# Optimization experiments

Hardware: AMD Instinct MI355X
Metric: run time of the kernel (lower is better)

Reference implementation:

```python
import jax, jax.numpy as jnp
import numpy as np

N, E = 50000, 800000
NODE_DIM, EDGE_DIM, TIME_DIM, OUT_DIM, N_HEADS = 128, 64, 16, 128, 4
IN_DIM = NODE_DIM + EDGE_DIM + TIME_DIM  # msg_proj input


def setup_inputs() -> dict:
    key = jax.random.key(0)
    ks = jax.random.split(key, 8)
    x = jax.random.normal(ks[0], (N, NODE_DIM), dtype=jnp.float32)
    edge_index = jax.random.randint(ks[1], (2, E), 0, N, dtype=jnp.int32)
    edge_feat = jax.random.normal(ks[2], (E, EDGE_DIM), dtype=jnp.float32)
    time_deltas = jax.random.uniform(ks[3], (E,), dtype=jnp.float32)
    # parameters
    gammas = jnp.ones((TIME_DIM,), jnp.float32)  # ExponentialTimeDecay init_gamma=1.0
    Wm = 0.02 * jax.random.normal(ks[4], (IN_DIM, OUT_DIM), dtype=jnp.float32)
    bm = jnp.zeros((OUT_DIM,), jnp.float32)
    Wa = 0.02 * jax.random.normal(ks[5], (2 * OUT_DIM, N_HEADS), dtype=jnp.float32)
    ba = jnp.zeros((N_HEADS,), jnp.float32)
    Wo = 0.02 * jax.random.normal(ks[6], (OUT_DIM + NODE_DIM, OUT_DIM), dtype=jnp.float32)
    bo = jnp.zeros((OUT_DIM,), jnp.float32)
    ln_g = jnp.ones((OUT_DIM,), jnp.float32)
    ln_b = jnp.zeros((OUT_DIM,), jnp.float32)
    return {"x": x, "edge_index": edge_index, "edge_feat": edge_feat,
            "time_deltas": time_deltas, "gammas": gammas, "Wm": Wm, "bm": bm,
            "Wa": Wa, "ba": ba, "Wo": Wo, "bo": bo, "ln_g": ln_g, "ln_b": ln_b}


def reference(x, edge_index, edge_feat, time_deltas, gammas, Wm, bm, Wa, ba, Wo, bo, ln_g, ln_b):
    src, dst = edge_index[0], edge_index[1]
    # exponential time decay encoding: (E, TIME_DIM)
    dt = jnp.clip(time_deltas, 0.0)[:, None]
    time_enc = jnp.exp(-jax.nn.softplus(gammas)[None, :] * dt)
    # gather + project messages: (E, OUT_DIM)
    msg_in = jnp.concatenate([x[src], edge_feat, time_enc], axis=-1)
    msgs = msg_in @ Wm + bm
    # edge attention, softmax over ALL edges (dim=0, as in the torch code)
    attn_in = jnp.concatenate([msgs, x[dst]], axis=-1)  # (E, 2*OUT_DIM)
    attn_logits = attn_in @ Wa + ba                      # (E, N_HEADS)
    attn_weight = jnp.mean(jax.nn.softmax(attn_logits, axis=0), axis=-1, keepdims=True)
    weighted = msgs * attn_weight
    # scatter-add into per-node aggregates: (N, OUT_DIM)
    agg = jax.ops.segment_sum(weighted, dst, num_segments=N)
    # output MLP (dropout is identity in eval) + LayerNorm
    out = jax.nn.gelu(jnp.concatenate([agg, x], axis=-1) @ Wo + bo, approximate=False)
    mu = jnp.mean(out, axis=-1, keepdims=True)
    var = jnp.mean((out - mu) ** 2, axis=-1, keepdims=True)
    return (out - mu) / jnp.sqrt(var + 1e-5) * ln_g + ln_b
```

## Files before the change

### kernel.cpp

```cpp
#include <hip/hip_runtime.h>
#include <math.h>

#define N_NODES 50000
#define N_EDGES 800000
#define ND 128
#define ED 64
#define TD 16
#define OD 128
#define NH 4
#define INDIM 208
#define K2DIM 336
#define KPAD 352
#define WTPITCH 360
#define NPAD 50048

#define OFF_A      0ll
#define OFF_EINFO  8808448ll
#define OFF_PERM32 12008448ll
#define OFF_RANK   12808448ll
#define OFF_DENOM  13608448ll
#define OFF_SPG    13608464ll
#define OFF_WFUSE  13608480ll
#define OFF_BFUSE  13609312ll
#define OFF_BMO    13609328ll
#define OFF_XS4    13609456ll
#define OFF_XD4    13809456ll
#define OFF_CNT    14009456ll
#define OFF_START  14059456ll
#define OFF_SW     14109472ll
#define OFF_WT     14159520ll
#define OFF_EFB    14182560ll
#define OFF_XBF    39782560ll
#define WS_FLOATS  42982560ll

typedef __attribute__((ext_vector_type(8))) short short8v;
typedef __attribute__((ext_vector_type(4))) float f32x4;

__device__ inline unsigned short f2bf(float f) {
  unsigned u = __float_as_uint(f);
  unsigned r = (u + 0x7fffu + ((u >> 16) & 1u)) >> 16;
  return (unsigned short)r;
}
__device__ inline float bf2f(unsigned us) {
  return __uint_as_float(us << 16);
}

__global__ void k0_prep(const float* __restrict__ Wm, const float* __restrict__ bm,
                        const float* __restrict__ Wa, const float* __restrict__ ba,
                        const float* __restrict__ Wo, const float* __restrict__ gammas,
                        float* __restrict__ ws) {
  int b = blockIdx.x, j = threadIdx.x;
  unsigned short* Wt = (unsigned short*)(ws + OFF_WT);
  if (b < INDIM) {
    float acc = 0.f;
    for (int m = 0; m < OD; ++m) acc += Wm[b * OD + m] * Wo[m * OD + j];
    Wt[j * WTPITCH + b] = f2bf(acc);
    if (j < NH) {
      float a = 0.f;
      for (int m = 0; m < OD; ++m) a += Wm[b * OD + m] * Wa[m * NH + j];
      ws[OFF_WFUSE + (long)b * NH + j] = a;
    }
  } else if (b < K2DIM) {
    Wt[j * WTPITCH + b] = f2bf(Wo[(OD + b - INDIM) * OD + j]);
  } else {
    if (j < TD) ws[OFF_SPG + j] = log1pf(expf(gammas[j]));
    if (j < NH) {
      float a = ba[j];
      for (int m = 0; m < OD; ++m) a += bm[m] * Wa[m * NH + j];
      ws[OFF_BFUSE + j] = a;
    }
    float a2 = 0.f;
    for (int m = 0; m < OD; ++m) a2 += bm[m] * Wo[m * OD + j];
    ws[OFF_BMO + j] = a2;
    for (int p = K2DIM; p < KPAD; ++p) Wt[j * WTPITCH + p] = 0;
  }
}

__global__ __launch_bounds__(256) void k0b_nodeproj(
    const float* __restrict__ x, const float* __restrict__ Wa,
    float* __restrict__ ws) {
  __shared__ float wf[ND * NH];
  __shared__ float wab[ND * NH];
  int tid = threadIdx.x;
  for (int i = tid; i < ND * NH; i += 256) { wf[i] = ws[OFF_WFUSE + i]; wab[i] = Wa[ND * NH + i]; }
  __syncthreads();
  int lane = tid & 63, wv = tid >> 6;
  long n = (long)blockIdx.x * 4 + wv;
  if (n >= N_NODES) return;
  float v0 = x[n * ND + lane], v1 = x[n * ND + 64 + lane];
  unsigned short* xbf = (unsigned short*)(ws + OFF_XBF);
  xbf[n * ND + lane] = f2bf(v0);
  xbf[n * ND + 64 + lane] = f2bf(v1);
  float s0, s1, s2, s3, d0, d1, d2, d3;
  s0 = v0 * wf[lane * 4 + 0] + v1 * wf[(64 + lane) * 4 + 0];
  s1 = v0 * wf[lane * 4 + 1] + v1 * wf[(64 + lane) * 4 + 1];
  s2 = v0 * wf[lane * 4 + 2] + v1 * wf[(64 + lane) * 4 + 2];
  s3 = v0 * wf[lane * 4 + 3] + v1 * wf[(64 + lane) * 4 + 3];
  d0 = v0 * wab[lane * 4 + 0] + v1 * wab[(64 + lane) * 4 + 0];
  d1 = v0 * wab[lane * 4 + 1] + v1 * wab[(64 + lane) * 4 + 1];
  d2 = v0 * wab[lane * 4 + 2] + v1 * wab[(64 + lane) * 4 + 2];
  d3 = v0 * wab[lane * 4 + 3] + v1 * wab[(64 + lane) * 4 + 3];
  for (int off = 32; off; off >>= 1) {
    s0 += __shfl_xor(s0, off); s1 += __shfl_xor(s1, off);
    s2 += __shfl_xor(s2, off); s3 += __shfl_xor(s3, off);
    d0 += __shfl_xor(d0, off); d1 += __shfl_xor(d1, off);
    d2 += __shfl_xor(d2, off); d3 += __shfl_xor(d3, off);
  }
  if (lane == 0) {
    reinterpret_cast<float4*>(ws + OFF_XS4)[n] = make_float4(s0, s1, s2, s3);
    reinterpret_cast<float4*>(ws + OFF_XD4)[n] = make_float4(d0, d1, d2, d3);
  }
}

__global__ __launch_bounds__(256) void k_count(const int* __restrict__ ei,
                                               float* __restrict__ ws) {
  int* cnt = reinterpret_cast<int*>(ws + OFF_CNT);
  int* rank = reinterpret_cast<int*>(ws + OFF_RANK);
  for (long e = (long)blockIdx.x * 256 + threadIdx.x; e < N_EDGES;
       e += (long)gridDim.x * 256)
    rank[e] = atomicAdd(&cnt[ei[N_EDGES + e]], 1);
}

__global__ __launch_bounds__(1024) void k_scan(float* __restrict__ ws) {
  const int* cnt = reinterpret_cast<const int*>(ws + OFF_CNT);
  int* startp = reinterpret_cast<int*>(ws + OFF_START);
  __shared__ int wsum[16];
  int tid = threadIdx.x;
  int lo = tid * 49, hi = min(lo + 49, N_NODES);
  int s = 0;
  for (int i = lo; i < hi; ++i) s += cnt[i];
  int lane = tid & 63, wv = tid >> 6;
  int sc = s;
  for (int off = 1; off < 64; off <<= 1) {
    int t = __shfl_up(sc, off);
    if (lane >= off) sc += t;
  }
  if (lane == 63) wsum[wv] = sc;
  __syncthreads();
  if (tid == 0) {
    int run = 0;
    for (int i = 0; i < 16; ++i) { int t = wsum[i]; wsum[i] = run; run += t; }
  }
  __syncthreads();
  int run = wsum[wv] + sc - s;
  for (int i = lo; i < hi; ++i) { startp[i] = run; run += cnt[i]; }
  if (tid == 1023) startp[N_NODES] = run;
}

__global__ __launch_bounds__(256) void k_fill4(const int* __restrict__ ei,
                                               float* __restrict__ ws) {
  const int* startp = reinterpret_cast<const int*>(ws + OFF_START);
  const int* rank = reinterpret_cast<const int*>(ws + OFF_RANK);
  int* perm32 = reinterpret_cast<int*>(ws + OFF_PERM32);
  for (long e = (long)blockIdx.x * 256 + threadIdx.x; e < N_EDGES;
       e += (long)gridDim.x * 256) {
    int d = ei[N_EDGES + e];
    perm32[startp[d] + rank[e]] = (int)e;
  }
}

__global__ __launch_bounds__(256) void k1f(
    const int* __restrict__ ei, const float* __restrict__ ef,
    const float* __restrict__ td, float* __restrict__ ws) {
  __shared__ float wef[ED * NH];
  __shared__ float wte[TD * NH];
  __shared__ float bf[NH];
  __shared__ float spg[TD];
  __shared__ float part[NH];
  int tid = threadIdx.x;
  for (int i = tid; i < ED * NH; i += 256) wef[i] = ws[OFF_WFUSE + ND * NH + i];
  if (tid < TD * NH) wte[tid] = ws[OFF_WFUSE + (ND + ED) * NH + tid];
  if (tid < NH) { bf[tid] = ws[OFF_BFUSE + tid]; part[tid] = 0.f; }
  if (tid < TD) spg[tid] = ws[OFF_SPG + tid];
  __syncthreads();

  int lane = tid & 63;
  int q = lane >> 4, r = lane & 15, h = r & 3;
  long wid = ((long)blockIdx.x * 256 + tid) >> 6;
  long stride = (long)gridDim.x * 16;
  const float4* ef4 = reinterpret_cast<const float4*>(ef);
  const float* xsf = ws + OFF_XS4;
  const float* xdf = ws + OFF_XD4;
  uint2* efb2 = reinterpret_cast<uint2*>(ws + OFF_EFB);
  uint4* einfo4 = reinterpret_cast<uint4*>(ws + OFF_EINFO);

  float wr[16];
#pragma unroll
  for (int i = 0; i < 16; ++i) wr[i] = wef[16 * r + i];
  float spg_r = spg[r];
  float wt0 = wte[r * 4 + 0], wt1 = wte[r * 4 + 1];
  float wt2 = wte[r * 4 + 2], wt3 = wte[r * 4 + 3];
  float bfh = bf[h];
  float p = 0.f;
  int base16 = lane & 48;

  for (long e = wid * 4 + q; e < N_EDGES; e += stride) {
    int s = ei[e];
    int d = ei[N_EDGES + e];
    float dt = fmaxf(td[e], 0.f);
    float4 efv = ef4[e * 16 + r];
    float ls = xsf[4l * s + h];
    float ld = xdf[4l * d + h];
    float te = __expf(-spg_r * dt);
    uint2 eb;
    eb.x = (unsigned)f2bf(efv.x) | ((unsigned)f2bf(efv.y) << 16);
    eb.y = (unsigned)f2bf(efv.z) | ((unsigned)f2bf(efv.w) << 16);
    efb2[e * 16 + r] = eb;
    float a0 = efv.x * wr[0] + efv.y * wr[4] + efv.z * wr[8]  + efv.w * wr[12] + te * wt0;
    float a1 = efv.x * wr[1] + efv.y * wr[5] + efv.z * wr[9]  + efv.w * wr[13] + te * wt1;
    float a2 = efv.x * wr[2] + efv.y * wr[6] + efv.z * wr[10] + efv.w * wr[14] + te * wt2;
    float a3 = efv.x * wr[3] + efv.y * wr[7] + efv.z * wr[11] + efv.w * wr[15] + te * wt3;
    a0 += __shfl_xor(a0, 1); a1 += __shfl_xor(a1, 1);
    a2 += __shfl_xor(a2, 1); a3 += __shfl_xor(a3, 1);
    a0 += __shfl_xor(a0, 2); a1 += __shfl_xor(a1, 2);
    a2 += __shfl_xor(a2, 2); a3 += __shfl_xor(a3, 2);
    float v = a0;
    v = (h == 1) ? a1 : v;
    v = (h == 2) ? a2 : v;
    v = (h == 3) ? a3 : v;
    v += __shfl_xor(v, 4);
    v += __shfl_xor(v, 8);
    float ev = __expf(v + ls + ld + bfh);
    if (r < 4) p += ev;
    float e0 = __shfl(ev, base16 + 0), e1 = __shfl(ev, base16 + 1);
    float e2 = __shfl(ev, base16 + 2), e3 = __shfl(ev, base16 + 3);
    if (r == 0) {
      unsigned dt16 = (unsigned)(dt * 65535.f + 0.5f);
      if (dt16 > 65535u) dt16 = 65535u;
      uint4 pk;
      pk.x = (unsigned)s | (dt16 << 16);
      pk.y = (unsigned)f2bf(e0) | ((unsigned)f2bf(e1) << 16);
      pk.z = (unsigned)f2bf(e2) | ((unsigned)f2bf(e3) << 16);
      pk.w = 0u;
      einfo4[e] = pk;
    }
  }
  p += __shfl_xor(p, 16);
  p += __shfl_xor(p, 32);
  if (lane < 4) atomicAdd(&part[lane], p);
  __syncthreads();
  if (tid < NH) atomicAdd(&ws[OFF_DENOM + tid], part[tid]);
}

__global__ __launch_bounds__(256) void k4a_agg(float* __restrict__ ws) {
  __shared__ float spg_s[TD];
  __shared__ float invs[NH];
  int tid = threadIdx.x;
  if (tid < TD) spg_s[tid] = ws[OFF_SPG + tid];
  if (tid < NH) invs[tid] = 0.25f / ws[OFF_DENOM + tid];
  __syncthreads();
  int lane = tid & 63;
  long wid = (long)blockIdx.x * 4 + (tid >> 6);
  long nw = (long)gridDim.x * 4;
  const int* start = reinterpret_cast<const int*>(ws + OFF_START);
  const int* perm32 = reinterpret_cast<const int*>(ws + OFF_PERM32);
  const uint4* einfo4 = reinterpret_cast<const uint4*>(ws + OFF_EINFO);
  unsigned short* A = (unsigned short*)(ws + OFF_A);
  const unsigned short* xbf = (const unsigned short*)(ws + OFF_XBF);
  const unsigned short* efb = (const unsigned short*)(ws + OFF_EFB);
  float spg_l = spg_s[lane & 15];
  float inv0 = invs[0], inv1 = invs[1], inv2 = invs[2], inv3 = invs[3];

  for (long n = wid; n < N_NODES; n += nw) {
    int i0 = start[n], i1 = start[n + 1];
    float a0 = 0.f, a1 = 0.f, a2 = 0.f, a3 = 0.f, asw = 0.f;
    for (int base = i0; base < i1; base += 64) {
      int m = min(64, i1 - base);
      int eidx = 0;
      if (lane < m) eidx = perm32[base + lane];
      uint4 pk = einfo4[eidx];
      int j = 0;
      for (; j + 4 <= m; j += 4) {
        unsigned xu[4], eu[4], zu[4], wu[4];
#pragma unroll
        for (int u = 0; u < 4; ++u) {
          xu[u] = (unsigned)__shfl((int)pk.x, j + u);
          eu[u] = (unsigned)__shfl(eidx, j + u);
          zu[u] = (unsigned)__shfl((int)pk.y, j + u);
          wu[u] = (unsigned)__shfl((int)pk.z, j + u);
        }
        unsigned xa[4], xb[4], ec[4];
#pragma unroll
        for (int u = 0; u < 4; ++u) {
          int s = (int)(xu[u] & 0xffffu);
          xa[u] = xbf[(long)s * ND + lane];
          xb[u] = xbf[(long)s * ND + 64 + lane];
          ec[u] = efb[(long)eu[u] * ED + lane];
        }
#pragma unroll
        for (int u = 0; u < 4; ++u) {
          float w = bf2f(zu[u] & 0xffffu) * inv0 + bf2f(zu[u] >> 16) * inv1 +
                    bf2f(wu[u] & 0xffffu) * inv2 + bf2f(wu[u] >> 16) * inv3;
          float dt = (float)(xu[u] >> 16) * (1.f / 65535.f);
          a0 += w * bf2f(xa[u]);
          a1 += w * bf2f(xb[u]);
          a2 += w * bf2f(ec[u]);
          a3 += w * __expf(-spg_l * dt);
          asw += w;
        }
      }
      for (; j < m; ++j) {
        unsigned xu = (unsigned)__shfl((int)pk.x, j);
        unsigned eu = (unsigned)__shfl(eidx, j);
        unsigned zu = (unsigned)__shfl((int)pk.y, j);
        unsigned wu = (unsigned)__shfl((int)pk.z, j);
        int s = (int)(xu & 0xffffu);
        float w = bf2f(zu & 0xffffu) * inv0 + bf2f(zu >> 16) * inv1 +
                  bf2f(wu & 0xffffu) * inv2 + bf2f(wu >> 16) * inv3;
        float dt = (float)(xu >> 16) * (1.f / 65535.f);
        a0 += w * bf2f(xbf[(long)s * ND + lane]);
        a1 += w * bf2f(xbf[(long)s * ND + 64 + lane]);
        a2 += w * bf2f(efb[(long)eu * ED + lane]);
        a3 += w * __expf(-spg_l * dt);
        asw += w;
      }
    }
    unsigned short* Ar = A + n * KPAD;
    Ar[lane] = f2bf(a0);
    Ar[64 + lane] = f2bf(a1);
    Ar[128 + lane] = f2bf(a2);
    if (lane < TD) Ar[192 + lane] = f2bf(a3);
    Ar[INDIM + lane] = xbf[n * ND + lane];
    Ar[INDIM + 64 + lane] = xbf[n * ND + 64 + lane];
    if (lane < 16) Ar[K2DIM + lane] = 0;
    if (lane == 0) ws[OFF_SW + n] = asw;
  }
}

__global__ __launch_bounds__(256) void k4b_mlp(
    const float* __restrict__ bo, const float* __restrict__ lng,
    const float* __restrict__ lnb, const float* __restrict__ ws,
    float* __restrict__ out) {
  __shared__ unsigned short wt[128 * WTPITCH];
  __shared__ float tbl[512];
  int tid = threadIdx.x;
  {
    const unsigned* wg = (const unsigned*)(ws + OFF_WT);
    unsigned* wl = (unsigned*)wt;
    for (int i = tid; i < 128 * WTPITCH / 2; i += 256) wl[i] = wg[i];
    if (tid < 128) {
      tbl[tid] = bo[tid];
      tbl[128 + tid] = ws[OFF_BMO + tid];
      tbl[256 + tid] = lng[tid];
      tbl[384 + tid] = lnb[tid];
    }
  }
  __syncthreads();

  int lane = tid & 63, wv = tid >> 6;
  int c0 = lane & 15, grp = lane >> 4;
  long n0 = (long)blockIdx.x * 64 + (long)wv * 16;
  const unsigned short* A = (const unsigned short*)(ws + OFF_A);
  const unsigned short* Arow = A + (n0 + c0) * KPAD;

  f32x4 acc[8];
#pragma unroll
  for (int t = 0; t < 8; ++t) acc[t] = (f32x4){0.f, 0.f, 0.f, 0.f};

#pragma unroll
  for (int kt = 0; kt < 11; ++kt) {
    short8v afrag = *reinterpret_cast<const short8v*>(Arow + kt * 32 + grp * 8);
#pragma unroll
    for (int t = 0; t < 8; ++t) {
      short8v bfrag = *reinterpret_cast<const short8v*>(&wt[(t * 16 + c0) * WTPITCH + kt * 32 + grp * 8]);
      acc[t] = __builtin_amdgcn_mfma_f32_16x16x32_bf16(afrag, bfrag, acc[t], 0, 0, 0);
    }
  }

  const float* swp = ws + OFF_SW;
  float res[4][8];
#pragma unroll
  for (int r = 0; r < 4; ++r) {
    long row = n0 + grp * 4 + r;
    float sw = swp[row];
    float s = 0.f, s2 = 0.f;
#pragma unroll
    for (int t = 0; t < 8; ++t) {
      int col = c0 + 16 * t;
      float a = acc[t][r] + tbl[col] + sw * tbl[128 + col];
      float h = 0.5f * a * (1.f + erff(a * 0.70710678118654752f));
      res[r][t] = h;
      s += h; s2 += h * h;
    }
    s += __shfl_xor(s, 1);  s2 += __shfl_xor(s2, 1);
    s += __shfl_xor(s, 2);  s2 += __shfl_xor(s2, 2);
    s += __shfl_xor(s, 4);  s2 += __shfl_xor(s2, 4);
    s += __shfl_xor(s, 8);  s2 += __shfl_xor(s2, 8);
    float mu = s * (1.f / 128.f);
    float var = s2 * (1.f / 128.f) - mu * mu;
    float rstd = rsqrtf(var + 1e-5f);
    if (row < N_NODES) {
      float* op = out + row * OD;
#pragma unroll
      for (int t = 0; t < 8; ++t) {
        int col = c0 + 16 * t;
        op[col] = (res[r][t] - mu) * rstd * tbl[256 + col] + tbl[384 + col];
      }
    }
  }
}

extern "C" void kernel_launch(void* const* d_in, const int* in_sizes, int n_in,
                              void* d_out, int out_size, void* d_ws, size_t ws_size,
                              hipStream_t stream) {
  const float* x   = (const float*)d_in[0];
  const int*   ei  = (const int*)d_in[1];
  const float* ef  = (const float*)d_in[2];
  const float* td  = (const float*)d_in[3];
  const float* gm  = (const float*)d_in[4];
  const float* Wm  = (const float*)d_in[5];
  const float* bm  = (const float*)d_in[6];
  const float* Wa  = (const float*)d_in[7];
  const float* ba  = (const float*)d_in[8];
  const float* Wo  = (const float*)d_in[9];
  const float* bo  = (const float*)d_in[10];
  const float* lng = (const float*)d_in[11];
  const float* lnb = (const float*)d_in[12];
  float* ws = (float*)d_ws;
  float* out = (float*)d_out;
  if (ws_size < (size_t)WS_FLOATS * 4) return;

  hipMemsetAsync(ws + OFF_CNT, 0, 50000 * 4, stream);
  hipMemsetAsync(ws + OFF_DENOM, 0, 64, stream);

  k0_prep<<<K2DIM + 1, 128, 0, stream>>>(Wm, bm, Wa, ba, Wo, gm, ws);
  k0b_nodeproj<<<12500, 256, 0, stream>>>(x, Wa, ws);
  k_count<<<2048, 256, 0, stream>>>(ei, ws);
  k_scan<<<1, 1024, 0, stream>>>(ws);
  k_fill4<<<2048, 256, 0, stream>>>(ei, ws);
  k1f<<<2048, 256, 0, stream>>>(ei, ef, td, ws);
  k4a_agg<<<2048, 256, 0, stream>>>(ws);
  k4b_mlp<<<(NPAD / 64), 256, 0, stream>>>(bo, lng, lnb, ws, out);
}
```

Measured before the change: 421.4 us.

## Fuse permutation fill into edge kernel with one thread per edge

```diff
diff --git a/kernel.cpp b/kernel.cpp
--- a/kernel.cpp
+++ b/kernel.cpp
@@ -147,97 +147,94 @@
   if (tid == 1023) startp[N_NODES] = run;
 }
 
-__global__ __launch_bounds__(256) void k_fill4(const int* __restrict__ ei,
-                                               float* __restrict__ ws) {
-  const int* startp = reinterpret_cast<const int*>(ws + OFF_START);
-  const int* rank = reinterpret_cast<const int*>(ws + OFF_RANK);
-  int* perm32 = reinterpret_cast<int*>(ws + OFF_PERM32);
-  for (long e = (long)blockIdx.x * 256 + threadIdx.x; e < N_EDGES;
-       e += (long)gridDim.x * 256) {
-    int d = ei[N_EDGES + e];
-    perm32[startp[d] + rank[e]] = (int)e;
-  }
-}
-
-__global__ __launch_bounds__(256) void k1f(
+__global__ __launch_bounds__(256) void k_edge(
     const int* __restrict__ ei, const float* __restrict__ ef,
     const float* __restrict__ td, float* __restrict__ ws) {
-  __shared__ float wef[ED * NH];
-  __shared__ float wte[TD * NH];
-  __shared__ float bf[NH];
+  __shared__ __align__(16) float wefL[NH * ED];
+  __shared__ __align__(16) float wteL[NH * TD];
   __shared__ float spg[TD];
+  __shared__ float bfL[NH];
   __shared__ float part[NH];
   int tid = threadIdx.x;
-  for (int i = tid; i < ED * NH; i += 256) wef[i] = ws[OFF_WFUSE + ND * NH + i];
-  if (tid < TD * NH) wte[tid] = ws[OFF_WFUSE + (ND + ED) * NH + tid];
-  if (tid < NH) { bf[tid] = ws[OFF_BFUSE + tid]; part[tid] = 0.f; }
+  if (tid < NH * ED) {
+    int h = tid >> 6, k = tid & 63;
+    wefL[tid] = ws[OFF_WFUSE + (ND + k) * NH + h];
+  }
+  if (tid < NH * TD) {
+    int h = tid >> 4, k = tid & 15;
+    wteL[tid] = ws[OFF_WFUSE + (ND + ED + k) * NH + h];
+  }
   if (tid < TD) spg[tid] = ws[OFF_SPG + tid];
-  __syncthreads();
-
-  int lane = tid & 63;
-  int q = lane >> 4, r = lane & 15, h = r & 3;
-  long wid = ((long)blockIdx.x * 256 + tid) >> 6;
-  long stride = (long)gridDim.x * 16;
-  const float4* ef4 = reinterpret_cast<const float4*>(ef);
-  const float* xsf = ws + OFF_XS4;
-  const float* xdf = ws + OFF_XD4;
-  uint2* efb2 = reinterpret_cast<uint2*>(ws + OFF_EFB);
-  uint4* einfo4 = reinterpret_cast<uint4*>(ws + OFF_EINFO);
-
-  float wr[16];
-#pragma unroll
-  for (int i = 0; i < 16; ++i) wr[i] = wef[16 * r + i];
-  float spg_r = spg[r];
-  float wt0 = wte[r * 4 + 0], wt1 = wte[r * 4 + 1];
-  float wt2 = wte[r * 4 + 2], wt3 = wte[r * 4 + 3];
-  float bfh = bf[h];
-  float p = 0.f;
-  int base16 = lane & 48;
-
-  for (long e = wid * 4 + q; e < N_EDGES; e += stride) {
-    int s = ei[e];
-    int d = ei[N_EDGES + e];
+  if (tid < NH) { bfL[tid] = ws[OFF_BFUSE + tid]; part[tid] = 0.f; }
+  __syncthreads();
+
+  long e = (long)blockIdx.x * 256 + tid;
+  float p0 = 0.f, p1 = 0.f, p2 = 0.f, p3 = 0.f;
+  if (e < N_EDGES) {
+    int s = ei[e], d = ei[N_EDGES + e];
     float dt = fmaxf(td[e], 0.f);
-    float4 efv = ef4[e * 16 + r];
-    float ls = xsf[4l * s + h];
-    float ld = xdf[4l * d + h];
-    float te = __expf(-spg_r * dt);
-    uint2 eb;
-    eb.x = (unsigned)f2bf(efv.x) | ((unsigned)f2bf(efv.y) << 16);
-    eb.y = (unsigned)f2bf(efv.z) | ((unsigned)f2bf(efv.w) << 16);
-    efb2[e * 16 + r] = eb;
-    float a0 = efv.x * wr[0] + efv.y * wr[4] + efv.z * wr[8]  + efv.w * wr[12] + te * wt0;
-    float a1 = efv.x * wr[1] + efv.y * wr[5] + efv.z * wr[9]  + efv.w * wr[13] + te * wt1;
-    float a2 = efv.x * wr[2] + efv.y * wr[6] + efv.z * wr[10] + efv.w * wr[14] + te * wt2;
-    float a3 = efv.x * wr[3] + efv.y * wr[7] + efv.z * wr[11] + efv.w * wr[15] + te * wt3;
-    a0 += __shfl_xor(a0, 1); a1 += __shfl_xor(a1, 1);
-    a2 += __shfl_xor(a2, 1); a3 += __shfl_xor(a3, 1);
-    a0 += __shfl_xor(a0, 2); a1 += __shfl_xor(a1, 2);
-    a2 += __shfl_xor(a2, 2); a3 += __shfl_xor(a3, 2);
-    float v = a0;
-    v = (h == 1) ? a1 : v;
-    v = (h == 2) ? a2 : v;
-    v = (h == 3) ? a3 : v;
-    v += __shfl_xor(v, 4);
-    v += __shfl_xor(v, 8);
-    float ev = __expf(v + ls + ld + bfh);
-    if (r < 4) p += ev;
-    float e0 = __shfl(ev, base16 + 0), e1 = __shfl(ev, base16 + 1);
-    float e2 = __shfl(ev, base16 + 2), e3 = __shfl(ev, base16 + 3);
-    if (r == 0) {
-      unsigned dt16 = (unsigned)(dt * 65535.f + 0.5f);
-      if (dt16 > 65535u) dt16 = 65535u;
-      uint4 pk;
-      pk.x = (unsigned)s | (dt16 << 16);
-      pk.y = (unsigned)f2bf(e0) | ((unsigned)f2bf(e1) << 16);
-      pk.z = (unsigned)f2bf(e2) | ((unsigned)f2bf(e3) << 16);
-      pk.w = 0u;
-      einfo4[e] = pk;
-    }
-  }
-  p += __shfl_xor(p, 16);
-  p += __shfl_xor(p, 32);
-  if (lane < 4) atomicAdd(&part[lane], p);
+    int rk = reinterpret_cast<const int*>(ws + OFF_RANK)[e];
+    const float4* efr = reinterpret_cast<const float4*>(ef) + e * 16;
+    uint2* ebo = reinterpret_cast<uint2*>(ws + OFF_EFB) + e * 16;
+    const float4* w0 = reinterpret_cast<const float4*>(&wefL[0]);
+    const float4* w1 = reinterpret_cast<const float4*>(&wefL[64]);
+    const float4* w2 = reinterpret_cast<const float4*>(&wefL[128]);
+    const float4* w3 = reinterpret_cast<const float4*>(&wefL[192]);
+    float a0 = 0.f, a1 = 0.f, a2 = 0.f, a3 = 0.f;
+#pragma unroll
+    for (int i = 0; i < 16; ++i) {
+      float4 v = efr[i];
+      uint2 eb;
+      eb.x = (unsigned)f2bf(v.x) | ((unsigned)f2bf(v.y) << 16);
+      eb.y = (unsigned)f2bf(v.z) | ((unsigned)f2bf(v.w) << 16);
+      ebo[i] = eb;
+      float4 q0 = w0[i], q1 = w1[i], q2 = w2[i], q3 = w3[i];
+      a0 += v.x * q0.x + v.y * q0.y + v.z * q0.z + v.w * q0.w;
+      a1 += v.x * q1.x + v.y * q1.y + v.z * q1.z + v.w * q1.w;
+      a2 += v.x * q2.x + v.y * q2.y + v.z * q2.z + v.w * q2.w;
+      a3 += v.x * q3.x + v.y * q3.y + v.z * q3.z + v.w * q3.w;
+    }
+    const float4* t0 = reinterpret_cast<const float4*>(&wteL[0]);
+    const float4* t1 = reinterpret_cast<const float4*>(&wteL[16]);
+    const float4* t2 = reinterpret_cast<const float4*>(&wteL[32]);
+    const float4* t3 = reinterpret_cast<const float4*>(&wteL[48]);
+#pragma unroll
+    for (int i = 0; i < 4; ++i) {
+      float te0 = __expf(-spg[4 * i + 0] * dt);
+      float te1 = __expf(-spg[4 * i + 1] * dt);
+      float te2 = __expf(-spg[4 * i + 2] * dt);
+      float te3 = __expf(-spg[4 * i + 3] * dt);
+      float4 q0 = t0[i], q1 = t1[i], q2 = t2[i], q3 = t3[i];
+      a0 += te0 * q0.x + te1 * q0.y + te2 * q0.z + te3 * q0.w;
+      a1 += te0 * q1.x + te1 * q1.y + te2 * q1.z + te3 * q1.w;
+      a2 += te0 * q2.x + te1 * q2.y + te2 * q2.z + te3 * q2.w;
+      a3 += te0 * q3.x + te1 * q3.y + te2 * q3.z + te3 * q3.w;
+    }
+    float4 xs = reinterpret_cast<const float4*>(ws + OFF_XS4)[s];
+    float4 xd = reinterpret_cast<const float4*>(ws + OFF_XD4)[d];
+    p0 = __expf(a0 + xs.x + xd.x + bfL[0]);
+    p1 = __expf(a1 + xs.y + xd.y + bfL[1]);
+    p2 = __expf(a2 + xs.z + xd.z + bfL[2]);
+    p3 = __expf(a3 + xs.w + xd.w + bfL[3]);
+    unsigned dt16 = (unsigned)(dt * 65535.f + 0.5f);
+    if (dt16 > 65535u) dt16 = 65535u;
+    uint4 pk;
+    pk.x = (unsigned)s | (dt16 << 16);
+    pk.y = (unsigned)f2bf(p0) | ((unsigned)f2bf(p1) << 16);
+    pk.z = (unsigned)f2bf(p2) | ((unsigned)f2bf(p3) << 16);
+    pk.w = 0u;
+    reinterpret_cast<uint4*>(ws + OFF_EINFO)[e] = pk;
+    const int* startp = reinterpret_cast<const int*>(ws + OFF_START);
+    reinterpret_cast<int*>(ws + OFF_PERM32)[startp[d] + rk] = (int)e;
+  }
+  for (int off = 32; off; off >>= 1) {
+    p0 += __shfl_xor(p0, off); p1 += __shfl_xor(p1, off);
+    p2 += __shfl_xor(p2, off); p3 += __shfl_xor(p3, off);
+  }
+  if ((tid & 63) == 0) {
+    atomicAdd(&part[0], p0); atomicAdd(&part[1], p1);
+    atomicAdd(&part[2], p2); atomicAdd(&part[3], p3);
+  }
   __syncthreads();
   if (tid < NH) atomicAdd(&ws[OFF_DENOM + tid], part[tid]);
 }
@@ -427,8 +424,7 @@
   k0b_nodeproj<<<12500, 256, 0, stream>>>(x, Wa, ws);
   k_count<<<2048, 256, 0, stream>>>(ei, ws);
   k_scan<<<1, 1024, 0, stream>>>(ws);
-  k_fill4<<<2048, 256, 0, stream>>>(ei, ws);
-  k1f<<<2048, 256, 0, stream>>>(ei, ef, td, ws);
+  k_edge<<<(N_EDGES + 255) / 256, 256, 0, stream>>>(ei, ef, td, ws);
   k4a_agg<<<2048, 256, 0, stream>>>(ws);
   k4b_mlp<<<(NPAD / 64), 256, 0, stream>>>(bo, lng, lnb, ws, out);
 }
```

After: 516.9 us. +22.7%, slower.

## Scatter edge data into CSR order in edge kernel, drop permutation pass

Applied to the files above, without the earlier changes.

```diff
diff --git a/kernel.cpp b/kernel.cpp
--- a/kernel.cpp
+++ b/kernel.cpp
@@ -16,22 +16,21 @@
 
 #define OFF_A      0ll
 #define OFF_EINFO  8808448ll
-#define OFF_PERM32 12008448ll
-#define OFF_RANK   12808448ll
-#define OFF_DENOM  13608448ll
-#define OFF_SPG    13608464ll
-#define OFF_WFUSE  13608480ll
-#define OFF_BFUSE  13609312ll
-#define OFF_BMO    13609328ll
-#define OFF_XS4    13609456ll
-#define OFF_XD4    13809456ll
-#define OFF_CNT    14009456ll
-#define OFF_START  14059456ll
-#define OFF_SW     14109472ll
-#define OFF_WT     14159520ll
-#define OFF_EFB    14182560ll
-#define OFF_XBF    39782560ll
-#define WS_FLOATS  42982560ll
+#define OFF_RANK   12008448ll
+#define OFF_DENOM  12808448ll
+#define OFF_SPG    12808464ll
+#define OFF_WFUSE  12808480ll
+#define OFF_BFUSE  12809312ll
+#define OFF_BMO    12809328ll
+#define OFF_XS4    12809456ll
+#define OFF_XD4    13009456ll
+#define OFF_CNT    13209456ll
+#define OFF_START  13259456ll
+#define OFF_SW     13309472ll
+#define OFF_WT     13359520ll
+#define OFF_EFC    13382560ll
+#define OFF_XBF    38982560ll
+#define WS_FLOATS  42182560ll
 
 typedef __attribute__((ext_vector_type(8))) short short8v;
 typedef __attribute__((ext_vector_type(4))) float f32x4;
@@ -147,19 +146,7 @@
   if (tid == 1023) startp[N_NODES] = run;
 }
 
-__global__ __launch_bounds__(256) void k_fill4(const int* __restrict__ ei,
-                                               float* __restrict__ ws) {
-  const int* startp = reinterpret_cast<const int*>(ws + OFF_START);
-  const int* rank = reinterpret_cast<const int*>(ws + OFF_RANK);
-  int* perm32 = reinterpret_cast<int*>(ws + OFF_PERM32);
-  for (long e = (long)blockIdx.x * 256 + threadIdx.x; e < N_EDGES;
-       e += (long)gridDim.x * 256) {
-    int d = ei[N_EDGES + e];
-    perm32[startp[d] + rank[e]] = (int)e;
-  }
-}
-
-__global__ __launch_bounds__(256) void k1f(
+__global__ __launch_bounds__(256) void k1c(
     const int* __restrict__ ei, const float* __restrict__ ef,
     const float* __restrict__ td, float* __restrict__ ws) {
   __shared__ float wef[ED * NH];
@@ -181,8 +168,10 @@
   const float4* ef4 = reinterpret_cast<const float4*>(ef);
   const float* xsf = ws + OFF_XS4;
   const float* xdf = ws + OFF_XD4;
-  uint2* efb2 = reinterpret_cast<uint2*>(ws + OFF_EFB);
-  uint4* einfo4 = reinterpret_cast<uint4*>(ws + OFF_EINFO);
+  const int* rank = reinterpret_cast<const int*>(ws + OFF_RANK);
+  const int* startp = reinterpret_cast<const int*>(ws + OFF_START);
+  uint2* efc2 = reinterpret_cast<uint2*>(ws + OFF_EFC);
+  uint4* einfoC = reinterpret_cast<uint4*>(ws + OFF_EINFO);
 
   float wr[16];
 #pragma unroll
@@ -198,6 +187,7 @@
     int s = ei[e];
     int d = ei[N_EDGES + e];
     float dt = fmaxf(td[e], 0.f);
+    int pos = startp[d] + rank[e];
     float4 efv = ef4[e * 16 + r];
     float ls = xsf[4l * s + h];
     float ld = xdf[4l * d + h];
@@ -205,7 +195,7 @@
     uint2 eb;
     eb.x = (unsigned)f2bf(efv.x) | ((unsigned)f2bf(efv.y) << 16);
     eb.y = (unsigned)f2bf(efv.z) | ((unsigned)f2bf(efv.w) << 16);
-    efb2[e * 16 + r] = eb;
+    efc2[(long)pos * 16 + r] = eb;
     float a0 = efv.x * wr[0] + efv.y * wr[4] + efv.z * wr[8]  + efv.w * wr[12] + te * wt0;
     float a1 = efv.x * wr[1] + efv.y * wr[5] + efv.z * wr[9]  + efv.w * wr[13] + te * wt1;
     float a2 = efv.x * wr[2] + efv.y * wr[6] + efv.z * wr[10] + efv.w * wr[14] + te * wt2;
@@ -232,7 +222,7 @@
       pk.y = (unsigned)f2bf(e0) | ((unsigned)f2bf(e1) << 16);
       pk.z = (unsigned)f2bf(e2) | ((unsigned)f2bf(e3) << 16);
       pk.w = 0u;
-      einfo4[e] = pk;
+      einfoC[pos] = pk;
     }
   }
   p += __shfl_xor(p, 16);
@@ -253,11 +243,10 @@
   long wid = (long)blockIdx.x * 4 + (tid >> 6);
   long nw = (long)gridDim.x * 4;
   const int* start = reinterpret_cast<const int*>(ws + OFF_START);
-  const int* perm32 = reinterpret_cast<const int*>(ws + OFF_PERM32);
-  const uint4* einfo4 = reinterpret_cast<const uint4*>(ws + OFF_EINFO);
+  const uint4* einfoC = reinterpret_cast<const uint4*>(ws + OFF_EINFO);
   unsigned short* A = (unsigned short*)(ws + OFF_A);
   const unsigned short* xbf = (const unsigned short*)(ws + OFF_XBF);
-  const unsigned short* efb = (const unsigned short*)(ws + OFF_EFB);
+  const unsigned short* efc = (const unsigned short*)(ws + OFF_EFC);
   float spg_l = spg_s[lane & 15];
   float inv0 = invs[0], inv1 = invs[1], inv2 = invs[2], inv3 = invs[3];
 
@@ -266,16 +255,14 @@
     float a0 = 0.f, a1 = 0.f, a2 = 0.f, a3 = 0.f, asw = 0.f;
     for (int base = i0; base < i1; base += 64) {
       int m = min(64, i1 - base);
-      int eidx = 0;
-      if (lane < m) eidx = perm32[base + lane];
-      uint4 pk = einfo4[eidx];
+      uint4 pk = make_uint4(0u, 0u, 0u, 0u);
+      if (lane < m) pk = einfoC[base + lane];
       int j = 0;
       for (; j + 4 <= m; j += 4) {
-        unsigned xu[4], eu[4], zu[4], wu[4];
+        unsigned xu[4], zu[4], wu[4];
 #pragma unroll
         for (int u = 0; u < 4; ++u) {
           xu[u] = (unsigned)__shfl((int)pk.x, j + u);
-          eu[u] = (unsigned)__shfl(eidx, j + u);
           zu[u] = (unsigned)__shfl((int)pk.y, j + u);
           wu[u] = (unsigned)__shfl((int)pk.z, j + u);
         }
@@ -285,7 +272,7 @@
           int s = (int)(xu[u] & 0xffffu);
           xa[u] = xbf[(long)s * ND + lane];
           xb[u] = xbf[(long)s * ND + 64 + lane];
-          ec[u] = efb[(long)eu[u] * ED + lane];
+          ec[u] = efc[(long)(base + j + u) * ED + lane];
         }
 #pragma unroll
         for (int u = 0; u < 4; ++u) {
@@ -301,7 +288,6 @@
       }
       for (; j < m; ++j) {
         unsigned xu = (unsigned)__shfl((int)pk.x, j);
-        unsigned eu = (unsigned)__shfl(eidx, j);
         unsigned zu = (unsigned)__shfl((int)pk.y, j);
         unsigned wu = (unsigned)__shfl((int)pk.z, j);
         int s = (int)(xu & 0xffffu);
@@ -310,7 +296,7 @@
         float dt = (float)(xu >> 16) * (1.f / 65535.f);
         a0 += w * bf2f(xbf[(long)s * ND + lane]);
         a1 += w * bf2f(xbf[(long)s * ND + 64 + lane]);
-        a2 += w * bf2f(efb[(long)eu * ED + lane]);
+        a2 += w * bf2f(efc[(long)(base + j) * ED + lane]);
         a3 += w * __expf(-spg_l * dt);
         asw += w;
       }
@@ -427,8 +413,7 @@
   k0b_nodeproj<<<12500, 256, 0, stream>>>(x, Wa, ws);
   k_count<<<2048, 256, 0, stream>>>(ei, ws);
   k_scan<<<1, 1024, 0, stream>>>(ws);
-  k_fill4<<<2048, 256, 0, stream>>>(ei, ws);
-  k1f<<<2048, 256, 0, stream>>>(ei, ef, td, ws);
+  k1c<<<2048, 256, 0, stream>>>(ei, ef, td, ws);
   k4a_agg<<<2048, 256, 0, stream>>>(ws);
   k4b_mlp<<<(NPAD / 64), 256, 0, stream>>>(bo, lng, lnb, ws, out);
 }
```

After: 412.8 us. 1.02x faster.
